# Kernel optimization log

Hardware: AMD Instinct MI355X
Metric: run time of the kernel (lower is better)

## Reference

```python
import jax, jax.numpy as jnp
import numpy as np

B, N, NEV, E, D, L = 4, 20000, 100000, 400000, 64, 3

def setup_inputs() -> dict:
    key = jax.random.key(0)
    ks = jax.random.split(key, 12)
    x = jax.random.normal(ks[0], (B, N, 3), dtype=jnp.float32)
    # channel 0 is the susceptible boolean mask (0/1)
    mask0 = (jax.random.uniform(ks[1], (B, N)) < 0.3).astype(jnp.float32)
    x = x.at[..., 0].set(mask0)
    dag_edge_index = jax.random.randint(ks[2], (2, E), 0, NEV, dtype=jnp.int64)
    event_to_node = jax.random.randint(ks[3], (NEV,), 0, N, dtype=jnp.int64)
    event_src_node = jax.random.randint(ks[4], (NEV,), 0, N, dtype=jnp.int64)
    s = 1.0 / np.sqrt(D)
    Wp = jax.random.normal(ks[5], (6, D), dtype=jnp.float32) * (1.0 / np.sqrt(6))
    bp = jnp.zeros((D,), dtype=jnp.float32)
    Ws = jax.random.normal(ks[6], (L, D, D), dtype=jnp.float32) * s
    Wa = jax.random.normal(ks[7], (L, D, D), dtype=jnp.float32) * s
    ba = jnp.zeros((L, D), dtype=jnp.float32)
    Wo = jax.random.normal(ks[8], (D,), dtype=jnp.float32) * s
    bo = jnp.zeros((), dtype=jnp.float32)
    return {"x": x, "Wp": Wp, "bp": bp, "Ws": Ws, "Wa": Wa, "ba": ba,
            "Wo": Wo, "bo": bo, "dag_edge_index": dag_edge_index,
            "event_to_node": event_to_node, "event_src_node": event_src_node}

def reference(x, Wp, bp, Ws, Wa, ba, Wo, bo, dag_edge_index, event_to_node, event_src_node):
    n_events = event_src_node.shape[0]
    # event features: [B, n_events, 6] -> project -> ReLU
    ev_feat = jnp.concatenate([x[:, event_src_node, :], x[:, event_to_node, :]], axis=-1)
    h = jax.nn.relu(ev_feat @ Wp + bp)  # [B, n_events, D]
    # reversed DAG edges: src = dag[1], dst = dag[0]
    src_e, dst_e = dag_edge_index[1], dag_edge_index[0]
    deg = jnp.zeros((n_events,), h.dtype).at[dst_e].add(1.0)
    deg = jnp.maximum(deg, 1.0)[None, :, None]
    for l in range(Ws.shape[0]):
        agg = jnp.zeros_like(h).at[:, dst_e].add(h[:, src_e])  # scatter-add mean agg
        h = jax.nn.relu(h @ Ws[l] + (agg / deg) @ Wa[l] + ba[l])
    # aggregate events back to nodes (mean)
    node_emb = jnp.zeros((x.shape[0], x.shape[1], h.shape[-1]), h.dtype).at[:, event_to_node].add(h)
    count = jnp.zeros((x.shape[1],), h.dtype).at[event_to_node].add(1.0)
    node_emb = node_emb / jnp.maximum(count, 1.0)[None, :, None]
    scores = node_emb @ Wo + bo  # [B, N]
    susceptible = x[..., 0] > 0
    scores = jnp.where(susceptible, -jnp.inf, scores)
    return jax.nn.log_softmax(scores, axis=-1)
```

## Files before the change

kernel.cpp:

```cpp
#include <hip/hip_runtime.h>
#include <hip/hip_bf16.h>
#include <math.h>

constexpr int B   = 4;
constexpr int N   = 20000;
constexpr int NEV = 100000;
constexpr int E   = 400000;
constexpr int D   = 64;
constexpr int L   = 3;
constexpr int CAP = 32;
constexpr int CHUNK = 625;
constexpr size_t HBYTES = (size_t)B * NEV * D + 256;

typedef short  short8 __attribute__((ext_vector_type(8)));
typedef float  f32x4  __attribute__((ext_vector_type(4)));
typedef float  f32x2  __attribute__((ext_vector_type(2)));


__device__ inline unsigned short f2bu(float f) {
  union { __hip_bfloat16 b; unsigned short s; } u;
  u.b = __float2bfloat16(f);
  return u.s;
}
__device__ inline unsigned packbf(float lo, float hi) {
  return ((unsigned)f2bu(hi) << 16) | (unsigned)f2bu(lo);
}
__device__ inline void cvt16(float* a, uint4 v) {
  unsigned vv[4] = {v.x, v.y, v.z, v.w};
#pragma unroll
  for (int i = 0; i < 4; ++i) {
    f32x2 lo = __builtin_amdgcn_cvt_pk_f32_fp8((int)vv[i], false);
    f32x2 hi = __builtin_amdgcn_cvt_pk_f32_fp8((int)vv[i], true);
    a[4 * i + 0] = lo[0]; a[4 * i + 1] = lo[1];
    a[4 * i + 2] = hi[0]; a[4 * i + 3] = hi[1];
  }
}
__device__ inline void add16(float* a, uint4 v) {
  unsigned vv[4] = {v.x, v.y, v.z, v.w};
#pragma unroll
  for (int i = 0; i < 4; ++i) {
    f32x2 lo = __builtin_amdgcn_cvt_pk_f32_fp8((int)vv[i], false);
    f32x2 hi = __builtin_amdgcn_cvt_pk_f32_fp8((int)vv[i], true);
    a[4 * i + 0] += lo[0]; a[4 * i + 1] += lo[1];
    a[4 * i + 2] += hi[0]; a[4 * i + 3] += hi[1];
  }
}
__device__ inline short8 pack8(const float* f) {
  union { unsigned u[4]; short8 s; } r;
#pragma unroll
  for (int i = 0; i < 4; ++i) r.u[i] = packbf(f[2 * i], f[2 * i + 1]);
  return r.s;
}
__device__ __forceinline__ void round4(const unsigned char* gb,
                                       const int* cr, int p, float* a) {
  int4 idx = *(const int4*)(cr + p);
  uint4 v0 = *(const uint4*)(gb + (size_t)idx.x * 256);
  uint4 v1 = *(const uint4*)(gb + (size_t)idx.y * 256);
  uint4 v2 = *(const uint4*)(gb + (size_t)idx.z * 256);
  uint4 v3 = *(const uint4*)(gb + (size_t)idx.w * 256);
  add16(a, v0); add16(a, v1); add16(a, v2); add16(a, v3);
}


__global__ void k_init(int4* __restrict__ ws4, int4* __restrict__ csrc4,
                       uint4* __restrict__ h0z, uint4* __restrict__ h1z) {
  int i = blockIdx.x * 256 + threadIdx.x;
  if (i < 30000) { ws4[i] = make_int4(0, 0, 0, 0); return; }
  int j = i - 30000;
  if (j < NEV * 4) {
    csrc4[(j >> 2) * 8 + (j & 3)] = make_int4(NEV, NEV, NEV, NEV);
    return;
  }
  int z = j - NEV * 4;
  if (z < 16) h0z[z] = make_uint4(0u, 0u, 0u, 0u);
  else if (z < 32) h1z[z - 16] = make_uint4(0u, 0u, 0u, 0u);
}

__global__ __launch_bounds__(256) void k_pp(
    const int* __restrict__ dag,
    int* __restrict__ cnt,
    int* __restrict__ csrc,
    const int* __restrict__ e2n,
    int* __restrict__ ncount,
    const float* __restrict__ Ws,
    const float* __restrict__ Wa,
    unsigned short* __restrict__ Wt,
    const float* __restrict__ x,
    const float* __restrict__ Wp,
    const float* __restrict__ bp,
    const int* __restrict__ esrc,
    unsigned* __restrict__ h,
    float* __restrict__ nscore) {
  int bid = blockIdx.x;
  if (bid < 391) {
    int i = bid * 256 + threadIdx.x;
    if (i < E / 4) {
      int4 d4 = ((const int4*)dag)[i];
      int4 s4 = ((const int4*)(dag + E))[i];
      int p0 = atomicAdd(&cnt[d4.x], 1);
      int p1 = atomicAdd(&cnt[d4.y], 1);
      int p2 = atomicAdd(&cnt[d4.z], 1);
      int p3 = atomicAdd(&cnt[d4.w], 1);
      if (p0 < CAP) csrc[d4.x * CAP + p0] = s4.x;
      if (p1 < CAP) csrc[d4.y * CAP + p1] = s4.y;
      if (p2 < CAP) csrc[d4.z * CAP + p2] = s4.z;
      if (p3 < CAP) csrc[d4.w * CAP + p3] = s4.w;
    }
    return;
  }
  if (bid < 489) {
    int i = (bid - 391) * 256 + threadIdx.x;
    if (i < NEV / 4) {
      int4 e4 = ((const int4*)e2n)[i];
      atomicAdd(&ncount[e4.x], 1);
      atomicAdd(&ncount[e4.y], 1);
      atomicAdd(&ncount[e4.z], 1);
      atomicAdd(&ncount[e4.w], 1);
    }
    return;
  }
  if (bid < 585) {
    int i = (bid - 489) * 256 + threadIdx.x;
    int l  = i >> 13;
    int r  = i & 8191;
    int n  = r >> 7;
    int s2 = r & 127;
    int hf = s2 >> 6, s = s2 & 63;
    int b  = ((s >> 3) & 3) * 16 + (s >> 5) * 8 + (s & 7);
    int c  = (b & 3) * 16 + (b >> 2);
    if (i < L * 64 * 128) {
      float v = hf ? Wa[l * 4096 + c * 64 + n]
                   : Ws[l * 4096 + c * 64 + n];
      Wt[l * 8192 + n * 128 + s2] = f2bu(v);
    }
    return;
  }
  int gid = (bid - 585) * 256 + threadIdx.x;
  if (gid < B * N) nscore[gid] = 0.f;
  const int lane  = threadIdx.x & 63;
  const int wvg   = gid >> 6;
  const int ebase = wvg * 4;
  const int ev = lane >> 4, bl = (lane >> 2) & 3, r = lane & 3;
  int sn = esrc[ebase + ev], tn = e2n[ebase + ev];
  float xval0 = (r < 3) ? x[(size_t)(bl * N + sn) * 3 + r]
                        : x[(size_t)(bl * N + tn) * 3];
  float xval1 = (r < 2) ? x[(size_t)(bl * N + tn) * 3 + 1 + r] : 0.f;
  const int base = lane & 60;
  float xv[6];
  xv[0] = __shfl(xval0, base + 0, 64);
  xv[1] = __shfl(xval0, base + 1, 64);
  xv[2] = __shfl(xval0, base + 2, 64);
  xv[3] = __shfl(xval0, base + 3, 64);
  xv[4] = __shfl(xval1, base + 0, 64);
  xv[5] = __shfl(xval1, base + 1, 64);
  const int p0 = (lane & 3) * 4;
  unsigned hv[4];
#pragma unroll
  for (int u = 0; u < 4; ++u) {
    int p = p0 + u;
    float a[4];
#pragma unroll
    for (int t = 0; t < 4; ++t) {
      int d = p + 16 * t;
      float acc = bp[d];
#pragma unroll
      for (int k = 0; k < 6; ++k) acc += xv[k] * Wp[k * 64 + d];
      a[t] = fmaxf(acc, 0.f);
    }
    int w = __builtin_amdgcn_cvt_pk_fp8_f32(a[0], a[1], 0, false);
    w     = __builtin_amdgcn_cvt_pk_fp8_f32(a[2], a[3], w, true);
    hv[u] = (unsigned)w;
  }
  *(uint4*)(h + (size_t)ebase * 64 + lane * 4) =
      make_uint4(hv[0], hv[1], hv[2], hv[3]);
}

template <bool LAST>
__global__ __launch_bounds__(256, 4) void k_layer(
    const unsigned short* __restrict__ Wt,
    const float* __restrict__ ba,
    const float* __restrict__ Wo,
    const int* __restrict__ e2n,
    const int* __restrict__ cnt,
    const int* __restrict__ csrc,
    const unsigned char* __restrict__ h_in,
    unsigned char* __restrict__ h_out,
    float* __restrict__ nscore) {
  const int tid  = threadIdx.x;
  const int wv   = tid >> 6, lane = tid & 63;
  const int e0   = blockIdx.x * 32;
  const int r0   = e0 * 4;
  const int m    = lane & 15, q = lane >> 4;
  const int el   = m >> 2;
  const int bb   = m & 3;
  const int eA   = e0 + wv * 4 + el;
  const int eB   = e0 + 16 + wv * 4 + el;

  const int* crA = csrc + (size_t)eA * CAP;
  const int* crB = csrc + (size_t)eB * CAP;
  int4 iA = *(const int4*)crA;
  int4 iB = *(const int4*)crB;
  uint4 vdA = *(const uint4*)(h_in + (size_t)(r0 + wv * 16 + m) * 64 + q * 16);
  uint4 vdB = *(const uint4*)(h_in + (size_t)(r0 + 64 + wv * 16 + m) * 64 + q * 16);
  int cA = cnt[eA];
  int cB = cnt[eB];

  const unsigned char* gb = h_in + bb * 64 + q * 16;
  float aA[16], aB[16];
#pragma unroll
  for (int i = 0; i < 16; ++i) { aA[i] = 0.f; aB[i] = 0.f; }
  {
    uint4 vA0 = *(const uint4*)(gb + (size_t)iA.x * 256);
    uint4 vA1 = *(const uint4*)(gb + (size_t)iA.y * 256);
    uint4 vA2 = *(const uint4*)(gb + (size_t)iA.z * 256);
    uint4 vA3 = *(const uint4*)(gb + (size_t)iA.w * 256);
    uint4 vB0 = *(const uint4*)(gb + (size_t)iB.x * 256);
    uint4 vB1 = *(const uint4*)(gb + (size_t)iB.y * 256);
    uint4 vB2 = *(const uint4*)(gb + (size_t)iB.z * 256);
    uint4 vB3 = *(const uint4*)(gb + (size_t)iB.w * 256);
    add16(aA, vA0); add16(aA, vA1); add16(aA, vA2); add16(aA, vA3);
    add16(aB, vB0); add16(aB, vB1); add16(aB, vB2); add16(aB, vB3);
  }
  int ccA = min(cA, CAP), ccA16 = min(ccA, 16);
  int ccB = min(cB, CAP), ccB16 = min(ccB, 16);
  for (int p = 4; p < ccA16; p += 4) round4(gb, crA, p, aA);
  for (int p = 4; p < ccB16; p += 4) round4(gb, crB, p, aB);
  for (int j = 16; j < ccA; ++j)
    add16(aA, *(const uint4*)(gb + (size_t)crA[j] * 256));
  for (int j = 16; j < ccB; ++j)
    add16(aB, *(const uint4*)(gb + (size_t)crB[j] * 256));
  {
    float invA = 1.f / fmaxf((float)cA, 1.f);
    float invB = 1.f / fmaxf((float)cB, 1.f);
#pragma unroll
    for (int i = 0; i < 16; ++i) { aA[i] *= invA; aB[i] *= invB; }
  }
  short8 agA0 = pack8(aA), agA1 = pack8(aA + 8);
  short8 agB0 = pack8(aB), agB1 = pack8(aB + 8);

  short8 adA0, adA1, adB0, adB1;
  {
    float f[16];
    cvt16(f, vdA); adA0 = pack8(f); adA1 = pack8(f + 8);
    cvt16(f, vdB); adB0 = pack8(f); adB1 = pack8(f + 8);
  }

  f32x4 accA[4], accB[4];
#pragma unroll
  for (int t = 0; t < 4; ++t) {
    float bv = ba[t * 16 + m];
    accA[t] = (f32x4){bv, bv, bv, bv};
    accB[t] = accA[t];
  }
  const unsigned short* wb = Wt + m * 128 + q * 8;
#pragma unroll
  for (int t = 0; t < 4; ++t) {
    short8 b0 = *(const short8*)(wb + t * 2048 + 0);
    short8 b1 = *(const short8*)(wb + t * 2048 + 32);
    short8 b2 = *(const short8*)(wb + t * 2048 + 64);
    short8 b3 = *(const short8*)(wb + t * 2048 + 96);
    accA[t] = __builtin_amdgcn_mfma_f32_16x16x32_bf16(adA0, b0, accA[t], 0, 0, 0);
    accA[t] = __builtin_amdgcn_mfma_f32_16x16x32_bf16(adA1, b1, accA[t], 0, 0, 0);
    accA[t] = __builtin_amdgcn_mfma_f32_16x16x32_bf16(agA0, b2, accA[t], 0, 0, 0);
    accA[t] = __builtin_amdgcn_mfma_f32_16x16x32_bf16(agA1, b3, accA[t], 0, 0, 0);
    accB[t] = __builtin_amdgcn_mfma_f32_16x16x32_bf16(adB0, b0, accB[t], 0, 0, 0);
    accB[t] = __builtin_amdgcn_mfma_f32_16x16x32_bf16(adB1, b1, accB[t], 0, 0, 0);
    accB[t] = __builtin_amdgcn_mfma_f32_16x16x32_bf16(agB0, b2, accB[t], 0, 0, 0);
    accB[t] = __builtin_amdgcn_mfma_f32_16x16x32_bf16(agB1, b3, accB[t], 0, 0, 0);
  }

  if constexpr (!LAST) {
#pragma unroll
    for (int g = 0; g < 2; ++g) {
      const f32x4* ac = g ? accB : accA;
#pragma unroll
      for (int r = 0; r < 4; ++r) {
        int w = __builtin_amdgcn_cvt_pk_fp8_f32(fmaxf(ac[0][r], 0.f),
                                                fmaxf(ac[1][r], 0.f), 0, false);
        w     = __builtin_amdgcn_cvt_pk_fp8_f32(fmaxf(ac[2][r], 0.f),
                                                fmaxf(ac[3][r], 0.f), w, true);
        int grow = r0 + g * 64 + wv * 16 + q * 4 + r;
        ((unsigned*)h_out)[grow * 16 + m] = (unsigned)w;
      }
    }
  } else {
    float w0 = Wo[m], w1 = Wo[16 + m], w2 = Wo[32 + m], w3 = Wo[48 + m];
#pragma unroll
    for (int g = 0; g < 2; ++g) {
      const f32x4* ac = g ? accB : accA;
#pragma unroll
      for (int r = 0; r < 4; ++r) {
        float v = fmaxf(ac[0][r], 0.f) * w0 + fmaxf(ac[1][r], 0.f) * w1
                + fmaxf(ac[2][r], 0.f) * w2 + fmaxf(ac[3][r], 0.f) * w3;
        v += __shfl_xor(v, 1, 64);
        v += __shfl_xor(v, 2, 64);
        v += __shfl_xor(v, 4, 64);
        v += __shfl_xor(v, 8, 64);
        if (m == 0) {
          int grow = r0 + g * 64 + wv * 16 + q * 4 + r;
          int e = grow >> 2, b = grow & 3;
          atomicAdd(&nscore[b * N + e2n[e]], v);
        }
      }
    }
  }
}

__device__ inline float ls_score(const float* nscore, const int* ncount,
                                 const float* x, float bov, int b, int n) {
  return (x[(size_t)(b * N + n) * 3] > 0.f)
             ? -INFINITY
             : nscore[b * N + n] / fmaxf((float)ncount[n], 1.f) + bov;
}

__global__ __launch_bounds__(256) void k_ls1(const float* __restrict__ nscore,
                                             const int* __restrict__ ncount,
                                             const float* __restrict__ x,
                                             const float* __restrict__ bo,
                                             float* __restrict__ pmax,
                                             float* __restrict__ psum,
                                             float* __restrict__ sc) {
  const int b = blockIdx.x >> 5, ch = blockIdx.x & 31;
  const int n0 = ch * CHUNK;
  const int tid = threadIdx.x;
  const float bov = bo[0];
  float s0 = -INFINITY, s1 = -INFINITY, s2 = -INFINITY;
  if (tid < CHUNK) {
    s0 = ls_score(nscore, ncount, x, bov, b, n0 + tid);
    sc[b * N + n0 + tid] = s0;
  }
  if (tid + 256 < CHUNK) {
    s1 = ls_score(nscore, ncount, x, bov, b, n0 + tid + 256);
    sc[b * N + n0 + tid + 256] = s1;
  }
  if (tid + 512 < CHUNK) {
    s2 = ls_score(nscore, ncount, x, bov, b, n0 + tid + 512);
    sc[b * N + n0 + tid + 512] = s2;
  }
  float m = fmaxf(fmaxf(s0, s1), s2);
  __shared__ float red[4];
#pragma unroll
  for (int o = 32; o; o >>= 1) m = fmaxf(m, __shfl_xor(m, o, 64));
  if ((tid & 63) == 0) red[tid >> 6] = m;
  __syncthreads();
  float pm = fmaxf(fmaxf(red[0], red[1]), fmaxf(red[2], red[3]));
  float pm2 = (pm == -INFINITY) ? 0.f : pm;
  float e = expf(s0 - pm2) + expf(s1 - pm2) + expf(s2 - pm2);
#pragma unroll
  for (int o = 32; o; o >>= 1) e += __shfl_xor(e, o, 64);
  __syncthreads();
  if ((tid & 63) == 0) red[tid >> 6] = e;
  __syncthreads();
  if (tid == 0) {
    pmax[blockIdx.x] = pm;
    psum[blockIdx.x] = red[0] + red[1] + red[2] + red[3];
  }
}

__global__ __launch_bounds__(256) void k_ls3(const float* __restrict__ pmax,
                                             const float* __restrict__ psum,
                                             const float* __restrict__ sc,
                                             float* __restrict__ out) {
  const int b = blockIdx.x >> 5, ch = blockIdx.x & 31;
  const int n0 = ch * CHUNK;
  const int tid = threadIdx.x;
  __shared__ float sgm, slse;
  if (tid < 64) {
    float pm = (tid < 32) ? pmax[b * 32 + tid] : -INFINITY;
    float ps = (tid < 32) ? psum[b * 32 + tid] : 0.f;
    float gm = pm;
#pragma unroll
    for (int o = 32; o; o >>= 1) gm = fmaxf(gm, __shfl_xor(gm, o, 64));
    float gm2 = (gm == -INFINITY) ? 0.f : gm;
    float c = (pm == -INFINITY) ? 0.f : ps * expf(pm - gm2);
#pragma unroll
    for (int o = 32; o; o >>= 1) c += __shfl_xor(c, o, 64);
    if (tid == 0) { sgm = gm; slse = logf(c); }
  }
  __syncthreads();
  const float gm = sgm, lse = slse;
  for (int i = tid; i < CHUNK; i += 256) {
    int n = n0 + i;
    out[b * N + n] = fmaxf(sc[b * N + n] - gm - lse, -3.0e38f);
  }
}

extern "C" void kernel_launch(void* const* d_in, const int* in_sizes, int n_in,
                              void* d_out, int out_size, void* d_ws, size_t ws_size,
                              hipStream_t stream) {
  const float* x   = (const float*)d_in[0];
  const float* Wp  = (const float*)d_in[1];
  const float* bp  = (const float*)d_in[2];
  const float* Ws  = (const float*)d_in[3];
  const float* Wa  = (const float*)d_in[4];
  const float* ba  = (const float*)d_in[5];
  const float* Wo  = (const float*)d_in[6];
  const float* bo  = (const float*)d_in[7];
  const int*   dag = (const int*)d_in[8];
  const int*   e2n = (const int*)d_in[9];
  const int*   esr = (const int*)d_in[10];

  int*   ws     = (int*)d_ws;
  int*   cnt    = ws;
  int*   ncount = ws + 100000;
  float* nscore = (float*)(ws + 120000);
  float* pmax   = (float*)(ws + 200000);
  float* psum   = (float*)(ws + 200128);
  int*   csrc   = ws + 200704;
  unsigned short* Wt = (unsigned short*)(ws + 3400704);
  unsigned char* h0 = (unsigned char*)(ws + 3406912);
  unsigned char* h1 = h0 + HBYTES;
  float* sc     = (float*)(h1 + HBYTES);
  float* out    = (float*)d_out;

  k_init<<<(30000 + NEV * 4 + 32 + 255) / 256, 256, 0, stream>>>(
      (int4*)ws, (int4*)csrc,
      (uint4*)(h0 + (size_t)NEV * 256), (uint4*)(h1 + (size_t)NEV * 256));
  k_pp<<<585 + NEV / 16, 256, 0, stream>>>(
      dag, cnt, csrc, e2n, ncount, Ws, Wa, Wt,
      x, Wp, bp, esr, (unsigned*)h0, nscore);

  k_layer<false><<<NEV / 32, 256, 0, stream>>>(Wt,         ba,       Wo, e2n,
                                               cnt, csrc, h0, h1, nscore);
  k_layer<false><<<NEV / 32, 256, 0, stream>>>(Wt + 8192,  ba + D,   Wo, e2n,
                                               cnt, csrc, h1, h0, nscore);
  k_layer<true><<<NEV / 32, 256, 0, stream>>>(Wt + 16384,  ba + 2*D, Wo, e2n,
                                              cnt, csrc, h0, h1, nscore);

  k_ls1<<<B * 32, 256, 0, stream>>>(nscore, ncount, x, bo, pmax, psum, sc);
  k_ls3<<<B * 32, 256, 0, stream>>>(pmax, psum, sc, out);
}
```

Before: 285.1 us.

## Partition events by in-degree so layer blocks process uniform-degree events

Adds a partition kernel that builds a permutation placing events with degree at most four at the front and the rest at the back, using atomic counters. Each layer kernel then handles events in permuted order, so a wavefront's events have similar neighbor counts and less divergence in the gather loop. The cost is an extra kernel launch, an indirect perm lookup, and scattered rather than contiguous h reads and writes, which may reduce coalescing.

```diff
diff --git a/kernel.cpp b/kernel.cpp
--- a/kernel.cpp
+++ b/kernel.cpp
@@ -63,8 +63,10 @@
 
 
 __global__ void k_init(int4* __restrict__ ws4, int4* __restrict__ csrc4,
+                       int* __restrict__ ctr,
                        uint4* __restrict__ h0z, uint4* __restrict__ h1z) {
   int i = blockIdx.x * 256 + threadIdx.x;
+  if (i == 0) { ctr[0] = 0; ctr[1] = 0; }
   if (i < 30000) { ws4[i] = make_int4(0, 0, 0, 0); return; }
   int j = i - 30000;
   if (j < NEV * 4) {
@@ -175,6 +177,19 @@
       make_uint4(hv[0], hv[1], hv[2], hv[3]);
 }
 
+__global__ void k_part(const int* __restrict__ cnt, int* __restrict__ ctr,
+                       int* __restrict__ perm) {
+  int i = blockIdx.x * 256 + threadIdx.x;
+  if (i >= NEV / 4) return;
+  int4 c4 = ((const int4*)cnt)[i];
+  int e = i * 4;
+  int p0 = (c4.x <= 4) ? atomicAdd(&ctr[0], 1) : NEV - 1 - atomicAdd(&ctr[1], 1);
+  int p1 = (c4.y <= 4) ? atomicAdd(&ctr[0], 1) : NEV - 1 - atomicAdd(&ctr[1], 1);
+  int p2 = (c4.z <= 4) ? atomicAdd(&ctr[0], 1) : NEV - 1 - atomicAdd(&ctr[1], 1);
+  int p3 = (c4.w <= 4) ? atomicAdd(&ctr[0], 1) : NEV - 1 - atomicAdd(&ctr[1], 1);
+  perm[p0] = e; perm[p1] = e + 1; perm[p2] = e + 2; perm[p3] = e + 3;
+}
+
 template <bool LAST>
 __global__ __launch_bounds__(256, 4) void k_layer(
     const unsigned short* __restrict__ Wt,
@@ -183,25 +198,25 @@
     const int* __restrict__ e2n,
     const int* __restrict__ cnt,
     const int* __restrict__ csrc,
+    const int* __restrict__ perm,
     const unsigned char* __restrict__ h_in,
     unsigned char* __restrict__ h_out,
     float* __restrict__ nscore) {
   const int tid  = threadIdx.x;
   const int wv   = tid >> 6, lane = tid & 63;
   const int e0   = blockIdx.x * 32;
-  const int r0   = e0 * 4;
   const int m    = lane & 15, q = lane >> 4;
   const int el   = m >> 2;
   const int bb   = m & 3;
-  const int eA   = e0 + wv * 4 + el;
-  const int eB   = e0 + 16 + wv * 4 + el;
+  const int eA   = perm[e0 + wv * 4 + el];
+  const int eB   = perm[e0 + 16 + wv * 4 + el];
 
   const int* crA = csrc + (size_t)eA * CAP;
   const int* crB = csrc + (size_t)eB * CAP;
   int4 iA = *(const int4*)crA;
   int4 iB = *(const int4*)crB;
-  uint4 vdA = *(const uint4*)(h_in + (size_t)(r0 + wv * 16 + m) * 64 + q * 16);
-  uint4 vdB = *(const uint4*)(h_in + (size_t)(r0 + 64 + wv * 16 + m) * 64 + q * 16);
+  uint4 vdA = *(const uint4*)(h_in + (size_t)(eA * 4 + bb) * 64 + q * 16);
+  uint4 vdB = *(const uint4*)(h_in + (size_t)(eB * 4 + bb) * 64 + q * 16);
   int cA = cnt[eA];
   int cB = cnt[eB];
 
@@ -269,18 +284,20 @@
     accB[t] = __builtin_amdgcn_mfma_f32_16x16x32_bf16(agB1, b3, accB[t], 0, 0, 0);
   }
 
+  const int peA = perm[e0 + wv * 4 + q];
+  const int peB = perm[e0 + 16 + wv * 4 + q];
   if constexpr (!LAST) {
 #pragma unroll
     for (int g = 0; g < 2; ++g) {
       const f32x4* ac = g ? accB : accA;
+      const int pe = g ? peB : peA;
 #pragma unroll
       for (int r = 0; r < 4; ++r) {
         int w = __builtin_amdgcn_cvt_pk_fp8_f32(fmaxf(ac[0][r], 0.f),
                                                 fmaxf(ac[1][r], 0.f), 0, false);
         w     = __builtin_amdgcn_cvt_pk_fp8_f32(fmaxf(ac[2][r], 0.f),
                                                 fmaxf(ac[3][r], 0.f), w, true);
-        int grow = r0 + g * 64 + wv * 16 + q * 4 + r;
-        ((unsigned*)h_out)[grow * 16 + m] = (unsigned)w;
+        ((unsigned*)h_out)[(pe * 4 + r) * 16 + m] = (unsigned)w;
       }
     }
   } else {
@@ -288,6 +305,7 @@
 #pragma unroll
     for (int g = 0; g < 2; ++g) {
       const f32x4* ac = g ? accB : accA;
+      const int pe = g ? peB : peA;
 #pragma unroll
       for (int r = 0; r < 4; ++r) {
         float v = fmaxf(ac[0][r], 0.f) * w0 + fmaxf(ac[1][r], 0.f) * w1
@@ -297,9 +315,7 @@
         v += __shfl_xor(v, 4, 64);
         v += __shfl_xor(v, 8, 64);
         if (m == 0) {
-          int grow = r0 + g * 64 + wv * 16 + q * 4 + r;
-          int e = grow >> 2, b = grow & 3;
-          atomicAdd(&nscore[b * N + e2n[e]], v);
+          atomicAdd(&nscore[r * N + e2n[pe]], v);
         }
       }
     }
@@ -406,26 +422,29 @@
   float* nscore = (float*)(ws + 120000);
   float* pmax   = (float*)(ws + 200000);
   float* psum   = (float*)(ws + 200128);
+  int*   ctr    = ws + 200260;
   int*   csrc   = ws + 200704;
   unsigned short* Wt = (unsigned short*)(ws + 3400704);
-  unsigned char* h0 = (unsigned char*)(ws + 3406912);
+  int*   perm   = ws + 3406912;
+  unsigned char* h0 = (unsigned char*)(ws + 3506944);
   unsigned char* h1 = h0 + HBYTES;
   float* sc     = (float*)(h1 + HBYTES);
   float* out    = (float*)d_out;
 
   k_init<<<(30000 + NEV * 4 + 32 + 255) / 256, 256, 0, stream>>>(
-      (int4*)ws, (int4*)csrc,
+      (int4*)ws, (int4*)csrc, ctr,
       (uint4*)(h0 + (size_t)NEV * 256), (uint4*)(h1 + (size_t)NEV * 256));
   k_pp<<<585 + NEV / 16, 256, 0, stream>>>(
       dag, cnt, csrc, e2n, ncount, Ws, Wa, Wt,
       x, Wp, bp, esr, (unsigned*)h0, nscore);
+  k_part<<<(NEV / 4 + 255) / 256, 256, 0, stream>>>(cnt, ctr, perm);
 
   k_layer<false><<<NEV / 32, 256, 0, stream>>>(Wt,         ba,       Wo, e2n,
-                                               cnt, csrc, h0, h1, nscore);
+                                               cnt, csrc, perm, h0, h1, nscore);
   k_layer<false><<<NEV / 32, 256, 0, stream>>>(Wt + 8192,  ba + D,   Wo, e2n,
-                                               cnt, csrc, h1, h0, nscore);
+                                               cnt, csrc, perm, h1, h0, nscore);
   k_layer<true><<<NEV / 32, 256, 0, stream>>>(Wt + 16384,  ba + 2*D, Wo, e2n,
-                                              cnt, csrc, h0, h1, nscore);
+                                              cnt, csrc, perm, h0, h1, nscore);
 
   k_ls1<<<B * 32, 256, 0, stream>>>(nscore, ncount, x, bo, pmax, psum, sc);
   k_ls3<<<B * 32, 256, 0, stream>>>(pmax, psum, sc, out);
```

After: 327.7 us. +15.0%, slower.
